# Kernel tuning notes

Hardware: AMD Instinct MI355X
Metric: run time of the kernel (lower is better)

The kernel has to match this reference:

```python
import jax, jax.numpy as jnp
import numpy as np

# structural constants (from dg config / init_kwargs)
B = 8192      # batch (L=1)
N = 64        # number of columns
C = 16        # one-hot width per column
D = N * C     # 1024
NUM = 32      # first NUM columns are numeric (use info['range'])
NCAUSAL = 16  # causal_cols = range(16)
K = 8         # info['range'][i] is [C, K]
HS = 1024
HP = 1024
TAU = 0.7
SMOOTH = 0.1  # kwargs['smoothing']


def setup_inputs() -> dict:
    key = jax.random.key(0)
    ks = jax.random.split(key, 20)
    s = 0.02
    inp = {
        'x': jax.random.uniform(ks[0], (B, D), dtype=jnp.float32),
        'truth_x': jax.random.normal(ks[1], (B, N), dtype=jnp.float32),
        # selector: Linear(D,HS) -> ReLU -> Linear(HS,N) -> Sigmoid
        'sel_w1': jax.random.normal(ks[2], (D, HS)) * s,
        'sel_b1': jnp.zeros((HS,), jnp.float32),
        'sel_w2': jax.random.normal(ks[3], (HS, N)) * s,
        'sel_b2': jnp.zeros((N,), jnp.float32),
        # perturber: D->HP->HP->HP->D with ReLU between
        'pw1': jax.random.normal(ks[4], (D, HP)) * s,
        'pb1': jnp.zeros((HP,), jnp.float32),
        'pw2': jax.random.normal(ks[5], (HP, HP)) * s,
        'pb2': jnp.zeros((HP,), jnp.float32),
        'pw3': jax.random.normal(ks[6], (HP, HP)) * s,
        'pb3': jnp.zeros((HP,), jnp.float32),
        'pw4': jax.random.normal(ks[7], (HP, D)) * s,
        'pb4': jnp.zeros((D,), jnp.float32),
        # dg.info['range'][i] for numeric columns: [NUM, C, K]
        'ranges': jax.random.normal(ks[8], (NUM, C, K), dtype=jnp.float32),
        # pre-drawn noise (training branch)
        'unif_a': jax.random.uniform(ks[9], (B, N), minval=1e-6, maxval=1.0 - 1e-6),
        'unif_b': jax.random.uniform(ks[10], (B, N), minval=1e-6, maxval=1.0 - 1e-6),
        'gumbel': jax.random.gumbel(ks[11], (B, N, C), dtype=jnp.float32),
    }
    return inp


def reference(x, truth_x, sel_w1, sel_b1, sel_w2, sel_b2,
              pw1, pb1, pw2, pb2, pw3, pb3, pw4, pb4,
              ranges, unif_a, unif_b, gumbel):
    # selector -> P in (0,1), shape [B, N]
    P = jax.nn.sigmoid(jax.nn.relu(x @ sel_w1 + sel_b1) @ sel_w2 + sel_b2)
    # relaxed Bernoulli (Sample_Bernoulli, training branch)
    ga = -jnp.log(-jnp.log(unif_a))
    gb = -jnp.log(-jnp.log(unif_b))
    no_logits = P * jnp.exp(ga) / TAU
    de_logits = no_logits + (1.0 - P) * jnp.exp(gb) / TAU
    probs = no_logits / de_logits                       # [B, N]
    # perturber MLP -> W, shape [B, D]
    h = jax.nn.relu(x @ pw1 + pb1)
    h = jax.nn.relu(h @ pw2 + pb2)
    h = jax.nn.relu(h @ pw3 + pb3)
    W = h @ pw4 + pb4
    # per-column blocks
    xr = x.reshape(B, N, C)
    logits = W.reshape(B, N, C)
    # data-dependent causal masking for causal columns
    curr = jnp.argmax(xr, axis=-1)                      # [B, N]
    causal = (jnp.arange(N) < NCAUSAL)[None, :, None]   # [1, N, 1]
    below = jnp.arange(C)[None, None, :] < curr[:, :, None]
    mask = jnp.where(causal & below, -100.0, jnp.where(causal, 1.0, 0.0))
    logits = logits + mask
    # label smoothing then Gumbel-softmax (soft), per Sample_Categorical
    pr = jax.nn.softmax(logits, axis=-1)
    pr = (1.0 - SMOOTH) * pr + SMOOTH / C
    logits = jnp.log(pr)
    y = jax.nn.softmax((logits + gumbel) / TAU, axis=-1)  # [B, N, C]
    # numeric columns: map categorical sample through range table, mix with truth
    xt_num = jnp.einsum('bnc,nck->bnk', y[:, :NUM], ranges).mean(axis=-1)  # [B, NUM]
    p_num = probs[:, :NUM]
    out_num = p_num * xt_num + (1.0 - p_num) * truth_x[:, :NUM]           # [B, NUM]
    # categorical columns: mix relaxed sample with original one-hot block
    p_cat = probs[:, NUM:, None]
    out_cat = p_cat * y[:, NUM:] + (1.0 - p_cat) * xr[:, NUM:]            # [B, N-NUM, C]
    xcf = jnp.concatenate([out_num, out_cat.reshape(B, (N - NUM) * C)], axis=1)
    return truth_x, xcf, P, W
```

## Files before the change

kernel.cpp:

```cpp
#include <hip/hip_runtime.h>
#include <hip/hip_bf16.h>
#include <cstdint>

#define B_DIM 8192
#define N_DIM 64
#define C_DIM 16
#define D_DIM 1024
#define NUM 32
#define NCAUSAL 16
#define K_RANGES 8
#define HS 1024
#define HP 1024
#define TAU 0.7f
#define SMOOTH 0.1f

typedef __bf16 bf16x8 __attribute__((ext_vector_type(8)));
typedef float f32x16 __attribute__((ext_vector_type(16)));

typedef const __attribute__((address_space(1))) uint32_t* gas_ptr;
typedef __attribute__((address_space(3))) uint32_t* las_ptr;

__device__ __forceinline__ void gld_lds16(const void* g, void* l) {
    __builtin_amdgcn_global_load_lds((gas_ptr)(uintptr_t)g,
                                     (las_ptr)(uint32_t)(uintptr_t)l,
                                     16, 0, 0);
}

__device__ __forceinline__ int swz(int r) { return (r & 3) ^ ((r >> 2) & 3); }

template <int ACT>
__device__ __forceinline__ void gemm_body2(
    const ushort* __restrict__ Ag, const ushort* __restrict__ Bg,
    const float* __restrict__ bias,
    float* __restrict__ Cf, __hip_bfloat16* __restrict__ Cb,
    int lda, int Nout, int ldC, int K, long m0, long n0,
    uint4 (*As)[512], uint4 (*Bs)[512])
{
    const int tid  = threadIdx.x;
    const int wave = tid >> 6;
    const int lane = tid & 63;
    const int wr = wave >> 1, wc = wave & 1;
    const int ln31 = lane & 31, blk = lane >> 5;

    f32x16 acc[2][2];
#pragma unroll
    for (int i = 0; i < 2; ++i)
#pragma unroll
        for (int j = 0; j < 2; ++j) acc[i][j] = (f32x16)(0.0f);

    const int c0 = wave * 128 + lane;
    const int c1 = wave * 128 + 64 + lane;

#define ISSUE_STAGE(buf, kt)                                                   \
    {                                                                          \
        int r0 = c0 >> 2, kc0 = (c0 & 3) ^ swz(r0);                            \
        int r1 = c1 >> 2, kc1 = (c1 & 3) ^ swz(r1);                            \
        gld_lds16(Ag + (m0 + r0) * (long)lda + (kt) + kc0 * 8,                 \
                  &As[buf][wave * 128]);                                       \
        gld_lds16(Bg + (n0 + r0) * (long)K + (kt) + kc0 * 8,                   \
                  &Bs[buf][wave * 128]);                                       \
        gld_lds16(Ag + (m0 + r1) * (long)lda + (kt) + kc1 * 8,                 \
                  &As[buf][wave * 128 + 64]);                                  \
        gld_lds16(Bg + (n0 + r1) * (long)K + (kt) + kc1 * 8,                   \
                  &Bs[buf][wave * 128 + 64]);                                  \
    }

    ISSUE_STAGE(0, 0);
    int cur = 0;
    for (int kt = 0; kt < K; kt += 32) {
        __syncthreads();
        if (kt + 32 < K) ISSUE_STAGE(cur ^ 1, kt + 32);

        bf16x8 af[2][2], bfr[2][2];
#pragma unroll
        for (int ks = 0; ks < 2; ++ks) {
            int ch = ks * 2 + blk;
#pragma unroll
            for (int mi = 0; mi < 2; ++mi) {
                int r = wr * 64 + mi * 32 + ln31;
                af[ks][mi] = __builtin_bit_cast(bf16x8, As[cur][r * 4 + (ch ^ swz(r))]);
            }
#pragma unroll
            for (int ni = 0; ni < 2; ++ni) {
                int n = wc * 64 + ni * 32 + ln31;
                bfr[ks][ni] = __builtin_bit_cast(bf16x8, Bs[cur][n * 4 + (ch ^ swz(n))]);
            }
        }
#pragma unroll
        for (int ks = 0; ks < 2; ++ks)
#pragma unroll
            for (int mi = 0; mi < 2; ++mi)
#pragma unroll
                for (int ni = 0; ni < 2; ++ni)
                    acc[mi][ni] = __builtin_amdgcn_mfma_f32_32x32x16_bf16(
                        af[ks][mi], bfr[ks][ni], acc[mi][ni], 0, 0, 0);
        cur ^= 1;
    }
#undef ISSUE_STAGE

    float bs2[2];
#pragma unroll
    for (int ni = 0; ni < 2; ++ni) {
        long col = n0 + wc * 64 + ni * 32 + ln31;
        bs2[ni] = (col < Nout && bias) ? bias[col] : 0.0f;
    }

#pragma unroll
    for (int mi = 0; mi < 2; ++mi) {
#pragma unroll
        for (int ni = 0; ni < 2; ++ni) {
            long col = n0 + wc * 64 + ni * 32 + ln31;
            if (col >= Nout) continue;
#pragma unroll
            for (int reg = 0; reg < 16; ++reg) {
                long row = m0 + wr * 64 + mi * 32 + (reg & 3) + 8 * (reg >> 2) + 4 * blk;
                float v = acc[mi][ni][reg] + bs2[ni];
                if (ACT == 1) {
                    v = fmaxf(v, 0.0f);
                    Cb[row * (long)ldC + col] = __float2bfloat16(v);
                } else if (ACT == 2) {
                    v = 1.0f / (1.0f + __expf(-v));
                    Cf[row * (long)ldC + col] = v;
                } else {
                    Cf[row * (long)ldC + col] = v;
                }
            }
        }
    }
}

template <int ACT>
__global__ __launch_bounds__(256, 2) void gemm_bt4(
    const __hip_bfloat16* __restrict__ A, const __hip_bfloat16* __restrict__ Bt,
    const float* __restrict__ bias,
    float* __restrict__ Cf, __hip_bfloat16* __restrict__ Cb,
    int lda, int Nout, int ldC, int K)
{
    __shared__ uint4 As[1024];
    __shared__ uint4 Bs[512];

    const ushort* Ag = (const ushort*)A;
    const ushort* Bg = (const ushort*)Bt;
    const long m0 = (long)blockIdx.y * 256;
    const long n0 = (long)blockIdx.x * 128;

    const int tid  = threadIdx.x;
    const int wave = tid >> 6;
    const int lane = tid & 63;
    const int wr = wave >> 1, wc = wave & 1;
    const int ln31 = lane & 31, blk = lane >> 5;

    f32x16 acc[4][2];
#pragma unroll
    for (int i = 0; i < 4; ++i)
#pragma unroll
        for (int j = 0; j < 2; ++j) acc[i][j] = (f32x16)(0.0f);

    for (int kt = 0; kt < K; kt += 32) {
#pragma unroll
        for (int r = 0; r < 4; ++r) {
            int s = r * 256 + tid;
            int row = s >> 2, ch = (s & 3) ^ swz(row);
            gld_lds16(Ag + (m0 + row) * (long)lda + kt + ch * 8,
                      &As[r * 256 + (wave << 6)]);
        }
#pragma unroll
        for (int r = 0; r < 2; ++r) {
            int s = r * 256 + tid;
            int row = s >> 2, ch = (s & 3) ^ swz(row);
            gld_lds16(Bg + (n0 + row) * (long)K + kt + ch * 8,
                      &Bs[r * 256 + (wave << 6)]);
        }
        __syncthreads();

        bf16x8 af[2][4], bfr[2][2];
#pragma unroll
        for (int ks = 0; ks < 2; ++ks) {
            int ch = ks * 2 + blk;
#pragma unroll
            for (int mi = 0; mi < 4; ++mi) {
                int r_ = wr * 128 + mi * 32 + ln31;
                af[ks][mi] = __builtin_bit_cast(bf16x8, As[r_ * 4 + (ch ^ swz(r_))]);
            }
#pragma unroll
            for (int ni = 0; ni < 2; ++ni) {
                int n_ = wc * 64 + ni * 32 + ln31;
                bfr[ks][ni] = __builtin_bit_cast(bf16x8, Bs[n_ * 4 + (ch ^ swz(n_))]);
            }
        }
#pragma unroll
        for (int ks = 0; ks < 2; ++ks)
#pragma unroll
            for (int mi = 0; mi < 4; ++mi)
#pragma unroll
                for (int ni = 0; ni < 2; ++ni)
                    acc[mi][ni] = __builtin_amdgcn_mfma_f32_32x32x16_bf16(
                        af[ks][mi], bfr[ks][ni], acc[mi][ni], 0, 0, 0);

        __syncthreads();
    }

    float bs2[2];
#pragma unroll
    for (int ni = 0; ni < 2; ++ni) {
        long col = n0 + wc * 64 + ni * 32 + ln31;
        bs2[ni] = (col < Nout && bias) ? bias[col] : 0.0f;
    }

#pragma unroll
    for (int mi = 0; mi < 4; ++mi) {
#pragma unroll
        for (int ni = 0; ni < 2; ++ni) {
            long col = n0 + wc * 64 + ni * 32 + ln31;
            if (col >= Nout) continue;
#pragma unroll
            for (int reg = 0; reg < 16; ++reg) {
                long row = m0 + wr * 128 + mi * 32 + (reg & 3) + 8 * (reg >> 2) + 4 * blk;
                float v = acc[mi][ni][reg] + bs2[ni];
                if (ACT == 1) {
                    v = fmaxf(v, 0.0f);
                    Cb[row * (long)ldC + col] = __float2bfloat16(v);
                } else if (ACT == 2) {
                    v = 1.0f / (1.0f + __expf(-v));
                    Cf[row * (long)ldC + col] = v;
                } else {
                    Cf[row * (long)ldC + col] = v;
                }
            }
        }
    }
}

template <int ACT>
__global__ __launch_bounds__(256, 2) void gemm_bt2(
    const __hip_bfloat16* __restrict__ A, const __hip_bfloat16* __restrict__ Bt,
    const float* __restrict__ bias,
    float* __restrict__ Cf, __hip_bfloat16* __restrict__ Cb,
    int lda, int Nout, int ldC, int K)
{
    __shared__ uint4 As[2][512];
    __shared__ uint4 Bs[2][512];
    gemm_body2<ACT>((const ushort*)A, (const ushort*)Bt, bias, Cf, Cb,
                    lda, Nout, ldC, K,
                    (long)blockIdx.y * 128, (long)blockIdx.x * 128, As, Bs);
}

__global__ __launch_bounds__(256, 2) void gemm_fused23(
    const __hip_bfloat16* __restrict__ act1,
    const __hip_bfloat16* __restrict__ p2t, const float* __restrict__ pb2,
    __hip_bfloat16* __restrict__ actB,
    const __hip_bfloat16* __restrict__ w2t, const float* __restrict__ sel_b2,
    float* __restrict__ outP)
{
    __shared__ uint4 As[2][512];
    __shared__ uint4 Bs[2][512];
    long m0 = (long)blockIdx.y * 128;
    if (blockIdx.x < 8) {
        gemm_body2<1>((const ushort*)(act1 + 1024), (const ushort*)p2t, pb2,
                      nullptr, actB, 2048, 1024, 1024, 1024,
                      m0, (long)blockIdx.x * 128, As, Bs);
    } else {
        gemm_body2<2>((const ushort*)act1, (const ushort*)w2t, sel_b2,
                      outP, nullptr, 2048, 64, 64, 1024,
                      m0, 0, As, Bs);
    }
}

struct PrepArgs {
    const float* src[6];
    __hip_bfloat16* dst[6];
    int Nsrc[6];
    int Npad[6];
    const float* ranges; float* rmean;
    const float* b1; const float* b2; float* bcat;
    const float* x; __hip_bfloat16* xbf;
};

__global__ void prep_kernel(PrepArgs a)
{
    int z = blockIdx.z;
    int tx = threadIdx.x, ty = threadIdx.y;
    int t = ty * 32 + tx;
    if (z == 7) {
        int bid = blockIdx.y * 32 + blockIdx.x;
        const float4* s4 = (const float4*)a.x;
        for (int i = bid * 256 + t; i < B_DIM * D_DIM / 4; i += 1024 * 256) {
            float4 v = s4[i];
            __hip_bfloat16* d = a.xbf + (size_t)i * 4;
            d[0] = __float2bfloat16(v.x);
            d[1] = __float2bfloat16(v.y);
            d[2] = __float2bfloat16(v.z);
            d[3] = __float2bfloat16(v.w);
        }
        return;
    }
    if (z == 6) {
        if (blockIdx.x || blockIdx.y) return;
        for (int j = t; j < NUM * C_DIM; j += 256) {
            float s = 0.0f;
#pragma unroll
            for (int k = 0; k < K_RANGES; ++k) s += a.ranges[j * K_RANGES + k];
            a.rmean[j] = s * (1.0f / K_RANGES);
        }
        for (int j = t; j < 1024; j += 256) {
            a.bcat[j]        = a.b1[j];
            a.bcat[1024 + j] = a.b2[j];
        }
        return;
    }
    const int Nsrc = a.Nsrc[z], Npad = a.Npad[z];
    int n0 = blockIdx.x * 32, k0 = blockIdx.y * 32;
    if (n0 >= Npad) return;
    const float* src = a.src[z];
    __hip_bfloat16* dst = a.dst[z];
    __shared__ float tile[32][33];
#pragma unroll
    for (int i = 0; i < 32; i += 8) {
        int k = k0 + ty + i, n = n0 + tx;
        tile[ty + i][tx] = (n < Nsrc) ? src[(size_t)k * Nsrc + n] : 0.0f;
    }
    __syncthreads();
#pragma unroll
    for (int i = 0; i < 32; i += 8) {
        int n = n0 + ty + i, k = k0 + tx;
        dst[(size_t)n * D_DIM + k] = __float2bfloat16(tile[tx][ty + i]);
    }
}

__global__ void finalize_kernel(
    const float* __restrict__ x, const float* __restrict__ truth,
    const float* __restrict__ ua, const float* __restrict__ ub,
    const float* __restrict__ gum, const float* __restrict__ rmean,
    const float* __restrict__ P, const float* __restrict__ W,
    float* __restrict__ out_truth, float* __restrict__ out_xcf)
{
    int idx = blockIdx.x * 256 + threadIdx.x;
    if (idx >= B_DIM * N_DIM) return;
    int b = idx >> 6, n = idx & 63;

    float tx = truth[idx];
    out_truth[idx] = tx;

    float p  = P[idx];
    float ea = -1.0f / logf(ua[idx]);
    float eb = -1.0f / logf(ub[idx]);
    float no = p * ea;
    float probs = no / (no + (1.0f - p) * eb);

    const float* Wrow = W + (size_t)idx * 16;
    const float* grow = gum + (size_t)idx * 16;
    float lo[16], g[16], xv[16];
#pragma unroll
    for (int c = 0; c < 16; c += 4) {
        float4 v = *(const float4*)(Wrow + c);
        lo[c] = v.x; lo[c + 1] = v.y; lo[c + 2] = v.z; lo[c + 3] = v.w;
        float4 gv = *(const float4*)(grow + c);
        g[c] = gv.x; g[c + 1] = gv.y; g[c + 2] = gv.z; g[c + 3] = gv.w;
    }

    bool needx = (n < NCAUSAL) || (n >= NUM);
    if (needx) {
        const float* xrow = x + (size_t)idx * 16;
#pragma unroll
        for (int c = 0; c < 16; c += 4) {
            float4 v = *(const float4*)(xrow + c);
            xv[c] = v.x; xv[c + 1] = v.y; xv[c + 2] = v.z; xv[c + 3] = v.w;
        }
    }

    if (n < NCAUSAL) {
        int curr = 0; float best = xv[0];
#pragma unroll
        for (int c = 1; c < 16; ++c)
            if (xv[c] > best) { best = xv[c]; curr = c; }
#pragma unroll
        for (int c = 0; c < 16; ++c) lo[c] += (c < curr) ? -100.0f : 1.0f;
    }

    float mx = lo[0];
#pragma unroll
    for (int c = 1; c < 16; ++c) mx = fmaxf(mx, lo[c]);
    float s = 0.0f, pr[16];
#pragma unroll
    for (int c = 0; c < 16; ++c) { pr[c] = __expf(lo[c] - mx); s += pr[c]; }
    float inv = 1.0f / s;
#pragma unroll
    for (int c = 0; c < 16; ++c)
        pr[c] = (1.0f - SMOOTH) * pr[c] * inv + (SMOOTH / C_DIM);

    float t[16];
    float mx2 = -1e30f;
#pragma unroll
    for (int c = 0; c < 16; ++c) {
        t[c] = (__logf(pr[c]) + g[c]) * (1.0f / TAU);
        mx2 = fmaxf(mx2, t[c]);
    }
    float s2 = 0.0f;
#pragma unroll
    for (int c = 0; c < 16; ++c) { t[c] = __expf(t[c] - mx2); s2 += t[c]; }
    float inv2 = 1.0f / s2;

    if (n < NUM) {
        float xt = 0.0f;
#pragma unroll
        for (int c = 0; c < 16; ++c) xt += t[c] * inv2 * rmean[n * 16 + c];
        out_xcf[(size_t)b * 544 + n] = probs * xt + (1.0f - probs) * tx;
    } else {
        float* o = out_xcf + (size_t)b * 544 + 32 + (size_t)(n - NUM) * 16;
#pragma unroll
        for (int c = 0; c < 16; ++c)
            o[c] = probs * t[c] * inv2 + (1.0f - probs) * xv[c];
    }
}

extern "C" void kernel_launch(void* const* d_in, const int* in_sizes, int n_in,
                              void* d_out, int out_size, void* d_ws, size_t ws_size,
                              hipStream_t stream)
{
    const float* x      = (const float*)d_in[0];
    const float* truth  = (const float*)d_in[1];
    const float* sel_w1 = (const float*)d_in[2];
    const float* sel_b1 = (const float*)d_in[3];
    const float* sel_w2 = (const float*)d_in[4];
    const float* sel_b2 = (const float*)d_in[5];
    const float* pw1    = (const float*)d_in[6];
    const float* pb1    = (const float*)d_in[7];
    const float* pw2    = (const float*)d_in[8];
    const float* pb2    = (const float*)d_in[9];
    const float* pw3    = (const float*)d_in[10];
    const float* pb3    = (const float*)d_in[11];
    const float* pw4    = (const float*)d_in[12];
    const float* pb4    = (const float*)d_in[13];
    const float* ranges = (const float*)d_in[14];
    const float* ua     = (const float*)d_in[15];
    const float* ub     = (const float*)d_in[16];
    const float* gum    = (const float*)d_in[17];

    float* out       = (float*)d_out;
    float* out_truth = out;
    float* out_xcf   = out + 524288;
    float* out_P     = out + 4980736;
    float* out_W     = out + 5505024;

    char* w = (char*)d_ws;
    size_t off = 0;
    __hip_bfloat16* A0   = (__hip_bfloat16*)(w + off); off += (size_t)B_DIM * D_DIM * 2;
    __hip_bfloat16* act1 = (__hip_bfloat16*)(w + off); off += (size_t)B_DIM * 2048 * 2;
    __hip_bfloat16* actB = (__hip_bfloat16*)(w + off); off += (size_t)B_DIM * HP * 2;
    __hip_bfloat16* actC = (__hip_bfloat16*)(w + off); off += (size_t)B_DIM * HP * 2;
    __hip_bfloat16* Wcat = (__hip_bfloat16*)(w + off); off += (size_t)2048 * D_DIM * 2;
    __hip_bfloat16* w2t  = (__hip_bfloat16*)(w + off); off += (size_t)128 * HS * 2;
    __hip_bfloat16* p2t  = (__hip_bfloat16*)(w + off); off += (size_t)HP * HP * 2;
    __hip_bfloat16* p3t  = (__hip_bfloat16*)(w + off); off += (size_t)HP * HP * 2;
    __hip_bfloat16* p4t  = (__hip_bfloat16*)(w + off); off += (size_t)D_DIM * HP * 2;
    float* rmean         = (float*)(w + off);          off += 512 * 4;
    float* bcat          = (float*)(w + off);          off += 2048 * 4;
    if (ws_size < off) return;

    PrepArgs pa;
    pa.src[0] = sel_w1; pa.dst[0] = Wcat;               pa.Nsrc[0] = HS;    pa.Npad[0] = 1024;
    pa.src[1] = pw1;    pa.dst[1] = Wcat + 1024 * 1024; pa.Nsrc[1] = HP;    pa.Npad[1] = 1024;
    pa.src[2] = sel_w2; pa.dst[2] = w2t;                pa.Nsrc[2] = N_DIM; pa.Npad[2] = 128;
    pa.src[3] = pw2;    pa.dst[3] = p2t;                pa.Nsrc[3] = HP;    pa.Npad[3] = 1024;
    pa.src[4] = pw3;    pa.dst[4] = p3t;                pa.Nsrc[4] = HP;    pa.Npad[4] = 1024;
    pa.src[5] = pw4;    pa.dst[5] = p4t;                pa.Nsrc[5] = D_DIM; pa.Npad[5] = 1024;
    pa.ranges = ranges; pa.rmean = rmean;
    pa.b1 = sel_b1; pa.b2 = pb1; pa.bcat = bcat;
    pa.x = x; pa.xbf = A0;

    prep_kernel<<<dim3(32, 32, 8), dim3(32, 8), 0, stream>>>(pa);

    gemm_bt4<1><<<dim3(16, 32), 256, 0, stream>>>(A0, Wcat, bcat, nullptr, act1,
                                                  D_DIM, 2048, 2048, D_DIM);
    gemm_fused23<<<dim3(9, 64), 256, 0, stream>>>(act1, p2t, pb2, actB, w2t, sel_b2, out_P);
    gemm_bt2<1><<<dim3(8, 64), 256, 0, stream>>>(actB, p3t, pb3, nullptr, actC,
                                                 HP, HP, HP, HP);
    gemm_bt2<0><<<dim3(8, 64), 256, 0, stream>>>(actC, p4t, pb4, out_W, nullptr,
                                                 HP, D_DIM, D_DIM, HP);

    finalize_kernel<<<(B_DIM * N_DIM + 255) / 256, 256, 0, stream>>>(
        x, truth, ua, ub, gum, rmean, out_P, out_W, out_truth, out_xcf);
}
```

Baseline: 303.5 us.

## Replace GEMM kernels with 256x256 8-wave pipelined GEMM and regroup selector layer

Replaces the separate 128/256-row GEMM kernels with a single 512-thread kernel that computes 256x256 tiles with K-step 64, an 8-chunk XOR swizzle, staged prefetch interleaved across four MFMA phases with explicit vmcnt waits, barriers and s_setprio, plus an XCD-aware block index swizzle. The selector second layer is moved from the layer-2 launch into the layer-3 launch as a second part, with its weight padding raised to 256 rows. The aim is higher data reuse per tile and better overlap of global-to-LDS loads with MFMA work. In exchange, grids shrink to 128-256 workgroups (wave quantization on many CUs), the tiles need more registers, and the padded selector part does wasted work.

```diff
diff --git a/kernel.cpp b/kernel.cpp
--- a/kernel.cpp
+++ b/kernel.cpp
@@ -26,244 +26,188 @@
                                      16, 0, 0);
 }
 
-__device__ __forceinline__ int swz(int r) { return (r & 3) ^ ((r >> 2) & 3); }
-
-template <int ACT>
-__device__ __forceinline__ void gemm_body2(
-    const ushort* __restrict__ Ag, const ushort* __restrict__ Bg,
-    const float* __restrict__ bias,
-    float* __restrict__ Cf, __hip_bfloat16* __restrict__ Cb,
-    int lda, int Nout, int ldC, int K, long m0, long n0,
-    uint4 (*As)[512], uint4 (*Bs)[512])
+struct G8Part {
+    const ushort* A; const ushort* B; const float* bias;
+    float* Cf; __hip_bfloat16* Cb;
+    int act, lda, Nout, ldC;
+};
+struct G8Args { G8Part p[2]; int K, split; };
+
+__device__ __forceinline__ void gemm8_body(
+    const G8Part& P, int K, long m0, long n0, uint4* lds)
 {
+    const ushort* __restrict__ Ag = P.A;
+    const ushort* __restrict__ Bg = P.B;
+    const int lda = P.lda;
+
     const int tid  = threadIdx.x;
     const int wave = tid >> 6;
     const int lane = tid & 63;
-    const int wr = wave >> 1, wc = wave & 1;
+    const int wr = wave >> 2, wcn = wave & 3;
     const int ln31 = lane & 31, blk = lane >> 5;
-
-    f32x16 acc[2][2];
-#pragma unroll
-    for (int i = 0; i < 2; ++i)
+    const int sl = (wave << 6) + lane;
+    const int nt = K >> 6;
+
+    uint4* Alds = lds;
+    uint4* Blds = lds + 4096;
+
+#define STAGE_A(buf, qoff, kt)                                                 \
+    {                                                                          \
+        _Pragma("unroll")                                                      \
+        for (int i_ = 0; i_ < 2; ++i_) {                                       \
+            int r_  = (i_ << 7) + (qoff) + (sl >> 3);                          \
+            int c_  = sl & 7;                                                  \
+            int gk_ = (kt) + ((c_ ^ (r_ & 7)) << 3);                           \
+            gld_lds16(Ag + (m0 + r_) * (long)lda + gk_,                        \
+                      Alds + (buf) * 2048 + (((i_ << 7) + (qoff)) << 3) +      \
+                          (wave << 6));                                        \
+        }                                                                      \
+    }
+#define STAGE_B(buf, h, kt)                                                    \
+    {                                                                          \
+        _Pragma("unroll")                                                      \
+        for (int i_ = 0; i_ < 2; ++i_) {                                       \
+            int r_  = ((h) << 7) + (i_ << 6) + (sl >> 3);                      \
+            int c_  = sl & 7;                                                  \
+            int gk_ = (kt) + ((c_ ^ (r_ & 7)) << 3);                           \
+            gld_lds16(Bg + (n0 + r_) * (long)K + gk_,                          \
+                      Blds + (buf) * 2048 + ((((h) << 7) + (i_ << 6)) << 3) +  \
+                          (wave << 6));                                        \
+        }                                                                      \
+    }
+#define LDA_F(buf, mi)                                                         \
+    _Pragma("unroll")                                                          \
+    for (int ks_ = 0; ks_ < 4; ++ks_) {                                        \
+        int r_ = wr * 128 + (mi) * 32 + ln31;                                  \
+        int c_ = (ks_ * 2 + blk) ^ (r_ & 7);                                   \
+        aF[ks_] = __builtin_bit_cast(bf16x8, Alds[(buf) * 2048 + r_ * 8 + c_]);\
+    }
+#define LDB_F(buf)                                                             \
+    _Pragma("unroll")                                                          \
+    for (int ni_ = 0; ni_ < 2; ++ni_) {                                        \
+        _Pragma("unroll")                                                      \
+        for (int ks_ = 0; ks_ < 4; ++ks_) {                                    \
+            int r_ = wcn * 64 + ni_ * 32 + ln31;                               \
+            int c_ = (ks_ * 2 + blk) ^ (r_ & 7);                               \
+            bF[ni_][ks_] =                                                     \
+                __builtin_bit_cast(bf16x8, Blds[(buf) * 2048 + r_ * 8 + c_]);  \
+        }                                                                      \
+    }
+#define PHASE_MFMA(mi)                                                         \
+    __builtin_amdgcn_s_barrier();                                              \
+    asm volatile("s_waitcnt lgkmcnt(0)");                                      \
+    __builtin_amdgcn_s_setprio(1);                                             \
+    _Pragma("unroll")                                                          \
+    for (int ks_ = 0; ks_ < 4; ++ks_) {                                        \
+        _Pragma("unroll")                                                      \
+        for (int ni_ = 0; ni_ < 2; ++ni_)                                      \
+            acc[mi][ni_] = __builtin_amdgcn_mfma_f32_32x32x16_bf16(            \
+                aF[ks_], bF[ni_][ks_], acc[mi][ni_], 0, 0, 0);                 \
+    }                                                                          \
+    __builtin_amdgcn_s_setprio(0);                                             \
+    __builtin_amdgcn_s_barrier();
+
+    STAGE_A(0, 0, 0);
+    STAGE_A(0, 64, 0);
+    STAGE_B(0, 0, 0);
+    STAGE_B(0, 1, 0);
+    STAGE_B(1, 0, 64);
+    STAGE_B(1, 1, 64);
+    STAGE_A(1, 0, 64);
+    asm volatile("s_waitcnt vmcnt(6)");
+    __builtin_amdgcn_s_barrier();
+
+    f32x16 acc[4][2];
+#pragma unroll
+    for (int i = 0; i < 4; ++i)
 #pragma unroll
         for (int j = 0; j < 2; ++j) acc[i][j] = (f32x16)(0.0f);
 
-    const int c0 = wave * 128 + lane;
-    const int c1 = wave * 128 + 64 + lane;
-
-#define ISSUE_STAGE(buf, kt)                                                   \
-    {                                                                          \
-        int r0 = c0 >> 2, kc0 = (c0 & 3) ^ swz(r0);                            \
-        int r1 = c1 >> 2, kc1 = (c1 & 3) ^ swz(r1);                            \
-        gld_lds16(Ag + (m0 + r0) * (long)lda + (kt) + kc0 * 8,                 \
-                  &As[buf][wave * 128]);                                       \
-        gld_lds16(Bg + (n0 + r0) * (long)K + (kt) + kc0 * 8,                   \
-                  &Bs[buf][wave * 128]);                                       \
-        gld_lds16(Ag + (m0 + r1) * (long)lda + (kt) + kc1 * 8,                 \
-                  &As[buf][wave * 128 + 64]);                                  \
-        gld_lds16(Bg + (n0 + r1) * (long)K + (kt) + kc1 * 8,                   \
-                  &Bs[buf][wave * 128 + 64]);                                  \
-    }
-
-    ISSUE_STAGE(0, 0);
-    int cur = 0;
-    for (int kt = 0; kt < K; kt += 32) {
-        __syncthreads();
-        if (kt + 32 < K) ISSUE_STAGE(cur ^ 1, kt + 32);
-
-        bf16x8 af[2][2], bfr[2][2];
-#pragma unroll
-        for (int ks = 0; ks < 2; ++ks) {
-            int ch = ks * 2 + blk;
-#pragma unroll
-            for (int mi = 0; mi < 2; ++mi) {
-                int r = wr * 64 + mi * 32 + ln31;
-                af[ks][mi] = __builtin_bit_cast(bf16x8, As[cur][r * 4 + (ch ^ swz(r))]);
-            }
-#pragma unroll
-            for (int ni = 0; ni < 2; ++ni) {
-                int n = wc * 64 + ni * 32 + ln31;
-                bfr[ks][ni] = __builtin_bit_cast(bf16x8, Bs[cur][n * 4 + (ch ^ swz(n))]);
-            }
-        }
-#pragma unroll
-        for (int ks = 0; ks < 2; ++ks)
-#pragma unroll
-            for (int mi = 0; mi < 2; ++mi)
-#pragma unroll
-                for (int ni = 0; ni < 2; ++ni)
-                    acc[mi][ni] = __builtin_amdgcn_mfma_f32_32x32x16_bf16(
-                        af[ks][mi], bfr[ks][ni], acc[mi][ni], 0, 0, 0);
-        cur ^= 1;
-    }
-#undef ISSUE_STAGE
-
+    for (int t = 0; t < nt; ++t) {
+        const int buf = t & 1;
+        bf16x8 aF[4], bF[2][4];
+
+        LDB_F(buf);
+        LDA_F(buf, 0);
+        if (t + 1 < nt) STAGE_A(buf ^ 1, 64, (t + 1) << 6);
+        PHASE_MFMA(0);
+
+        LDA_F(buf, 1);
+        if (t + 2 < nt) STAGE_B(buf, 0, (t + 2) << 6);
+        PHASE_MFMA(1);
+
+        LDA_F(buf, 2);
+        if (t + 2 < nt) STAGE_B(buf, 1, (t + 2) << 6);
+        PHASE_MFMA(2);
+
+        LDA_F(buf, 3);
+        if (t + 2 < nt) STAGE_A(buf, 0, (t + 2) << 6);
+        if (t < nt - 2) {
+            asm volatile("s_waitcnt vmcnt(6)");
+        } else if (t == nt - 2) {
+            asm volatile("s_waitcnt vmcnt(0)");
+        }
+        PHASE_MFMA(3);
+    }
+#undef STAGE_A
+#undef STAGE_B
+#undef LDA_F
+#undef LDB_F
+#undef PHASE_MFMA
+
+    const int act = P.act, Nout = P.Nout, ldC = P.ldC;
     float bs2[2];
 #pragma unroll
     for (int ni = 0; ni < 2; ++ni) {
-        long col = n0 + wc * 64 + ni * 32 + ln31;
-        bs2[ni] = (col < Nout && bias) ? bias[col] : 0.0f;
-    }
-
-#pragma unroll
-    for (int mi = 0; mi < 2; ++mi) {
+        long col = n0 + wcn * 64 + ni * 32 + ln31;
+        bs2[ni] = (col < Nout && P.bias) ? P.bias[col] : 0.0f;
+    }
+#pragma unroll
+    for (int mi = 0; mi < 4; ++mi) {
 #pragma unroll
         for (int ni = 0; ni < 2; ++ni) {
-            long col = n0 + wc * 64 + ni * 32 + ln31;
-            if (col >= Nout) continue;
-#pragma unroll
-            for (int reg = 0; reg < 16; ++reg) {
-                long row = m0 + wr * 64 + mi * 32 + (reg & 3) + 8 * (reg >> 2) + 4 * blk;
-                float v = acc[mi][ni][reg] + bs2[ni];
-                if (ACT == 1) {
-                    v = fmaxf(v, 0.0f);
-                    Cb[row * (long)ldC + col] = __float2bfloat16(v);
-                } else if (ACT == 2) {
-                    v = 1.0f / (1.0f + __expf(-v));
-                    Cf[row * (long)ldC + col] = v;
-                } else {
-                    Cf[row * (long)ldC + col] = v;
-                }
-            }
-        }
-    }
-}
-
-template <int ACT>
-__global__ __launch_bounds__(256, 2) void gemm_bt4(
-    const __hip_bfloat16* __restrict__ A, const __hip_bfloat16* __restrict__ Bt,
-    const float* __restrict__ bias,
-    float* __restrict__ Cf, __hip_bfloat16* __restrict__ Cb,
-    int lda, int Nout, int ldC, int K)
-{
-    __shared__ uint4 As[1024];
-    __shared__ uint4 Bs[512];
-
-    const ushort* Ag = (const ushort*)A;
-    const ushort* Bg = (const ushort*)Bt;
-    const long m0 = (long)blockIdx.y * 256;
-    const long n0 = (long)blockIdx.x * 128;
-
-    const int tid  = threadIdx.x;
-    const int wave = tid >> 6;
-    const int lane = tid & 63;
-    const int wr = wave >> 1, wc = wave & 1;
-    const int ln31 = lane & 31, blk = lane >> 5;
-
-    f32x16 acc[4][2];
-#pragma unroll
-    for (int i = 0; i < 4; ++i)
-#pragma unroll
-        for (int j = 0; j < 2; ++j) acc[i][j] = (f32x16)(0.0f);
-
-    for (int kt = 0; kt < K; kt += 32) {
-#pragma unroll
-        for (int r = 0; r < 4; ++r) {
-            int s = r * 256 + tid;
-            int row = s >> 2, ch = (s & 3) ^ swz(row);
-            gld_lds16(Ag + (m0 + row) * (long)lda + kt + ch * 8,
-                      &As[r * 256 + (wave << 6)]);
-        }
-#pragma unroll
-        for (int r = 0; r < 2; ++r) {
-            int s = r * 256 + tid;
-            int row = s >> 2, ch = (s & 3) ^ swz(row);
-            gld_lds16(Bg + (n0 + row) * (long)K + kt + ch * 8,
-                      &Bs[r * 256 + (wave << 6)]);
-        }
-        __syncthreads();
-
-        bf16x8 af[2][4], bfr[2][2];
-#pragma unroll
-        for (int ks = 0; ks < 2; ++ks) {
-            int ch = ks * 2 + blk;
-#pragma unroll
-            for (int mi = 0; mi < 4; ++mi) {
-                int r_ = wr * 128 + mi * 32 + ln31;
-                af[ks][mi] = __builtin_bit_cast(bf16x8, As[r_ * 4 + (ch ^ swz(r_))]);
-            }
-#pragma unroll
-            for (int ni = 0; ni < 2; ++ni) {
-                int n_ = wc * 64 + ni * 32 + ln31;
-                bfr[ks][ni] = __builtin_bit_cast(bf16x8, Bs[n_ * 4 + (ch ^ swz(n_))]);
-            }
-        }
-#pragma unroll
-        for (int ks = 0; ks < 2; ++ks)
-#pragma unroll
-            for (int mi = 0; mi < 4; ++mi)
-#pragma unroll
-                for (int ni = 0; ni < 2; ++ni)
-                    acc[mi][ni] = __builtin_amdgcn_mfma_f32_32x32x16_bf16(
-                        af[ks][mi], bfr[ks][ni], acc[mi][ni], 0, 0, 0);
-
-        __syncthreads();
-    }
-
-    float bs2[2];
-#pragma unroll
-    for (int ni = 0; ni < 2; ++ni) {
-        long col = n0 + wc * 64 + ni * 32 + ln31;
-        bs2[ni] = (col < Nout && bias) ? bias[col] : 0.0f;
-    }
-
-#pragma unroll
-    for (int mi = 0; mi < 4; ++mi) {
-#pragma unroll
-        for (int ni = 0; ni < 2; ++ni) {
-            long col = n0 + wc * 64 + ni * 32 + ln31;
+            long col = n0 + wcn * 64 + ni * 32 + ln31;
             if (col >= Nout) continue;
 #pragma unroll
             for (int reg = 0; reg < 16; ++reg) {
                 long row = m0 + wr * 128 + mi * 32 + (reg & 3) + 8 * (reg >> 2) + 4 * blk;
                 float v = acc[mi][ni][reg] + bs2[ni];
-                if (ACT == 1) {
+                if (act == 1) {
                     v = fmaxf(v, 0.0f);
-                    Cb[row * (long)ldC + col] = __float2bfloat16(v);
-                } else if (ACT == 2) {
+                    P.Cb[row * (long)ldC + col] = __float2bfloat16(v);
+                } else if (act == 2) {
                     v = 1.0f / (1.0f + __expf(-v));
-                    Cf[row * (long)ldC + col] = v;
+                    P.Cf[row * (long)ldC + col] = v;
                 } else {
-                    Cf[row * (long)ldC + col] = v;
+                    P.Cf[row * (long)ldC + col] = v;
                 }
             }
         }
     }
 }
 
-template <int ACT>
-__global__ __launch_bounds__(256, 2) void gemm_bt2(
-    const __hip_bfloat16* __restrict__ A, const __hip_bfloat16* __restrict__ Bt,
-    const float* __restrict__ bias,
-    float* __restrict__ Cf, __hip_bfloat16* __restrict__ Cb,
-    int lda, int Nout, int ldC, int K)
+__global__ __launch_bounds__(512, 2) void gemm8_k(G8Args g)
 {
-    __shared__ uint4 As[2][512];
-    __shared__ uint4 Bs[2][512];
-    gemm_body2<ACT>((const ushort*)A, (const ushort*)Bt, bias, Cf, Cb,
-                    lda, Nout, ldC, K,
-                    (long)blockIdx.y * 128, (long)blockIdx.x * 128, As, Bs);
-}
-
-__global__ __launch_bounds__(256, 2) void gemm_fused23(
-    const __hip_bfloat16* __restrict__ act1,
-    const __hip_bfloat16* __restrict__ p2t, const float* __restrict__ pb2,
-    __hip_bfloat16* __restrict__ actB,
-    const __hip_bfloat16* __restrict__ w2t, const float* __restrict__ sel_b2,
-    float* __restrict__ outP)
-{
-    __shared__ uint4 As[2][512];
-    __shared__ uint4 Bs[2][512];
-    long m0 = (long)blockIdx.y * 128;
-    if (blockIdx.x < 8) {
-        gemm_body2<1>((const ushort*)(act1 + 1024), (const ushort*)p2t, pb2,
-                      nullptr, actB, 2048, 1024, 1024, 1024,
-                      m0, (long)blockIdx.x * 128, As, Bs);
+    __shared__ uint4 lds[8192];
+    const int nwg = gridDim.x;
+    const int cpx = nwg >> 3;
+    const int bid = blockIdx.x;
+    const int swz = (bid & 7) * cpx + (bid >> 3);
+
+    long m0, n0;
+    int part;
+    if (swz < g.split) {
+        part = 0;
+        int ty = swz & 31;
+        int tx = swz >> 5;
+        m0 = (long)ty * 256;
+        n0 = (long)tx * 256;
     } else {
-        gemm_body2<2>((const ushort*)act1, (const ushort*)w2t, sel_b2,
-                      outP, nullptr, 2048, 64, 64, 1024,
-                      m0, 0, As, Bs);
-    }
+        part = 1;
+        m0 = (long)(swz - g.split) * 256;
+        n0 = 0;
+    }
+    gemm8_body(g.p[part], g.K, m0, n0, lds);
 }
 
 struct PrepArgs {
@@ -449,7 +393,7 @@
     __hip_bfloat16* actB = (__hip_bfloat16*)(w + off); off += (size_t)B_DIM * HP * 2;
     __hip_bfloat16* actC = (__hip_bfloat16*)(w + off); off += (size_t)B_DIM * HP * 2;
     __hip_bfloat16* Wcat = (__hip_bfloat16*)(w + off); off += (size_t)2048 * D_DIM * 2;
-    __hip_bfloat16* w2t  = (__hip_bfloat16*)(w + off); off += (size_t)128 * HS * 2;
+    __hip_bfloat16* w2t  = (__hip_bfloat16*)(w + off); off += (size_t)256 * HS * 2;
     __hip_bfloat16* p2t  = (__hip_bfloat16*)(w + off); off += (size_t)HP * HP * 2;
     __hip_bfloat16* p3t  = (__hip_bfloat16*)(w + off); off += (size_t)HP * HP * 2;
     __hip_bfloat16* p4t  = (__hip_bfloat16*)(w + off); off += (size_t)D_DIM * HP * 2;
@@ -460,7 +404,7 @@
     PrepArgs pa;
     pa.src[0] = sel_w1; pa.dst[0] = Wcat;               pa.Nsrc[0] = HS;    pa.Npad[0] = 1024;
     pa.src[1] = pw1;    pa.dst[1] = Wcat + 1024 * 1024; pa.Nsrc[1] = HP;    pa.Npad[1] = 1024;
-    pa.src[2] = sel_w2; pa.dst[2] = w2t;                pa.Nsrc[2] = N_DIM; pa.Npad[2] = 128;
+    pa.src[2] = sel_w2; pa.dst[2] = w2t;                pa.Nsrc[2] = N_DIM; pa.Npad[2] = 256;
     pa.src[3] = pw2;    pa.dst[3] = p2t;                pa.Nsrc[3] = HP;    pa.Npad[3] = 1024;
     pa.src[4] = pw3;    pa.dst[4] = p3t;                pa.Nsrc[4] = HP;    pa.Npad[4] = 1024;
     pa.src[5] = pw4;    pa.dst[5] = p4t;                pa.Nsrc[5] = D_DIM; pa.Npad[5] = 1024;
@@ -470,13 +414,36 @@
 
     prep_kernel<<<dim3(32, 32, 8), dim3(32, 8), 0, stream>>>(pa);
 
-    gemm_bt4<1><<<dim3(16, 32), 256, 0, stream>>>(A0, Wcat, bcat, nullptr, act1,
-                                                  D_DIM, 2048, 2048, D_DIM);
-    gemm_fused23<<<dim3(9, 64), 256, 0, stream>>>(act1, p2t, pb2, actB, w2t, sel_b2, out_P);
-    gemm_bt2<1><<<dim3(8, 64), 256, 0, stream>>>(actB, p3t, pb3, nullptr, actC,
-                                                 HP, HP, HP, HP);
-    gemm_bt2<0><<<dim3(8, 64), 256, 0, stream>>>(actC, p4t, pb4, out_W, nullptr,
-                                                 HP, D_DIM, D_DIM, HP);
+    {
+        G8Args g{};
+        g.p[0] = { (const ushort*)A0, (const ushort*)Wcat, bcat,
+                   nullptr, act1, 1, 1024, 2048, 2048 };
+        g.K = 1024; g.split = 256;
+        gemm8_k<<<256, 512, 0, stream>>>(g);
+    }
+    {
+        G8Args g{};
+        g.p[0] = { (const ushort*)(act1 + 1024), (const ushort*)p2t, pb2,
+                   nullptr, actB, 1, 2048, 1024, 1024 };
+        g.K = 1024; g.split = 128;
+        gemm8_k<<<128, 512, 0, stream>>>(g);
+    }
+    {
+        G8Args g{};
+        g.p[0] = { (const ushort*)actB, (const ushort*)p3t, pb3,
+                   nullptr, actC, 1, 1024, 1024, 1024 };
+        g.p[1] = { (const ushort*)act1, (const ushort*)w2t, sel_b2,
+                   out_P, nullptr, 2, 2048, 64, 64 };
+        g.K = 1024; g.split = 128;
+        gemm8_k<<<160, 512, 0, stream>>>(g);
+    }
+    {
+        G8Args g{};
+        g.p[0] = { (const ushort*)actC, (const ushort*)p4t, pb4,
+                   out_W, nullptr, 0, 1024, 1024, 1024 };
+        g.K = 1024; g.split = 128;
+        gemm8_k<<<128, 512, 0, stream>>>(g);
+    }
 
     finalize_kernel<<<(B_DIM * N_DIM + 255) / 256, 256, 0, stream>>>(
         x, truth, ua, ub, gum, rmean, out_P, out_W, out_truth, out_xcf);
```

Measured after the change: 360.1 us. +18.7%, slower.

## Use 8-wave 128x128 GEMM blocks with one load per thread per stage

Applied to the files above, without the earlier changes.

Rewrites the GEMM body so each 128x128 tile is computed by 8 waves, where each wave owns a 64x32 sub-tile, instead of 4 waves each owning 64x64. Each thread now issues a single A and B async load per stage, and the load addresses are precomputed once. The first GEMM switches from the 256x128 single-buffered kernel to this double-buffered 128x128 kernel. The aim is more resident waves per CU to hide latency, fewer accumulator registers, and cheaper address math. In exchange, each wave reuses its fragments less, so the LDS read traffic per MFMA goes up.

```diff
diff --git a/kernel.cpp b/kernel.cpp
--- a/kernel.cpp
+++ b/kernel.cpp
@@ -29,7 +29,7 @@
 __device__ __forceinline__ int swz(int r) { return (r & 3) ^ ((r >> 2) & 3); }
 
 template <int ACT>
-__device__ __forceinline__ void gemm_body2(
+__device__ __forceinline__ void gemm_body8(
     const ushort* __restrict__ Ag, const ushort* __restrict__ Bg,
     const float* __restrict__ bias,
     float* __restrict__ Cf, __hip_bfloat16* __restrict__ Cb,
@@ -38,91 +38,70 @@
 {
     const int tid  = threadIdx.x;
     const int wave = tid >> 6;
-    const int lane = tid & 63;
-    const int wr = wave >> 1, wc = wave & 1;
-    const int ln31 = lane & 31, blk = lane >> 5;
-
-    f32x16 acc[2][2];
-#pragma unroll
-    for (int i = 0; i < 2; ++i)
-#pragma unroll
-        for (int j = 0; j < 2; ++j) acc[i][j] = (f32x16)(0.0f);
-
-    const int c0 = wave * 128 + lane;
-    const int c1 = wave * 128 + 64 + lane;
-
-#define ISSUE_STAGE(buf, kt)                                                   \
+    const int ln31 = tid & 31, blk = (tid >> 5) & 1;
+    const int wr = wave >> 2, wc = wave & 3;
+
+    const int row = tid >> 2;
+    const int ch  = (tid & 3) ^ swz(row);
+    const ushort* aSrc = Ag + (m0 + row) * (long)lda + ch * 8;
+    const ushort* bSrc = Bg + (n0 + row) * (long)K   + ch * 8;
+    const int ldsOff = wave << 6;
+
+    f32x16 acc[2];
+    acc[0] = (f32x16)(0.0f);
+    acc[1] = (f32x16)(0.0f);
+
+#define ISSUE_STAGE8(buf, kt)                                                  \
     {                                                                          \
-        int r0 = c0 >> 2, kc0 = (c0 & 3) ^ swz(r0);                            \
-        int r1 = c1 >> 2, kc1 = (c1 & 3) ^ swz(r1);                            \
-        gld_lds16(Ag + (m0 + r0) * (long)lda + (kt) + kc0 * 8,                 \
-                  &As[buf][wave * 128]);                                       \
-        gld_lds16(Bg + (n0 + r0) * (long)K + (kt) + kc0 * 8,                   \
-                  &Bs[buf][wave * 128]);                                       \
-        gld_lds16(Ag + (m0 + r1) * (long)lda + (kt) + kc1 * 8,                 \
-                  &As[buf][wave * 128 + 64]);                                  \
-        gld_lds16(Bg + (n0 + r1) * (long)K + (kt) + kc1 * 8,                   \
-                  &Bs[buf][wave * 128 + 64]);                                  \
-    }
-
-    ISSUE_STAGE(0, 0);
+        gld_lds16(aSrc + (kt), &As[buf][ldsOff]);                              \
+        gld_lds16(bSrc + (kt), &Bs[buf][ldsOff]);                              \
+    }
+
+    ISSUE_STAGE8(0, 0);
     int cur = 0;
     for (int kt = 0; kt < K; kt += 32) {
         __syncthreads();
-        if (kt + 32 < K) ISSUE_STAGE(cur ^ 1, kt + 32);
-
-        bf16x8 af[2][2], bfr[2][2];
+        if (kt + 32 < K) ISSUE_STAGE8(cur ^ 1, kt + 32);
+
+        bf16x8 af[2][2], bfr[2];
 #pragma unroll
         for (int ks = 0; ks < 2; ++ks) {
-            int ch = ks * 2 + blk;
+            int c = ks * 2 + blk;
 #pragma unroll
             for (int mi = 0; mi < 2; ++mi) {
                 int r = wr * 64 + mi * 32 + ln31;
-                af[ks][mi] = __builtin_bit_cast(bf16x8, As[cur][r * 4 + (ch ^ swz(r))]);
+                af[ks][mi] = __builtin_bit_cast(bf16x8, As[cur][r * 4 + (c ^ swz(r))]);
             }
-#pragma unroll
-            for (int ni = 0; ni < 2; ++ni) {
-                int n = wc * 64 + ni * 32 + ln31;
-                bfr[ks][ni] = __builtin_bit_cast(bf16x8, Bs[cur][n * 4 + (ch ^ swz(n))]);
-            }
+            int n = wc * 32 + ln31;
+            bfr[ks] = __builtin_bit_cast(bf16x8, Bs[cur][n * 4 + (c ^ swz(n))]);
         }
 #pragma unroll
         for (int ks = 0; ks < 2; ++ks)
 #pragma unroll
             for (int mi = 0; mi < 2; ++mi)
-#pragma unroll
-                for (int ni = 0; ni < 2; ++ni)
-                    acc[mi][ni] = __builtin_amdgcn_mfma_f32_32x32x16_bf16(
-                        af[ks][mi], bfr[ks][ni], acc[mi][ni], 0, 0, 0);
+                acc[mi] = __builtin_amdgcn_mfma_f32_32x32x16_bf16(
+                    af[ks][mi], bfr[ks], acc[mi], 0, 0, 0);
         cur ^= 1;
     }
-#undef ISSUE_STAGE
-
-    float bs2[2];
-#pragma unroll
-    for (int ni = 0; ni < 2; ++ni) {
-        long col = n0 + wc * 64 + ni * 32 + ln31;
-        bs2[ni] = (col < Nout && bias) ? bias[col] : 0.0f;
-    }
-
-#pragma unroll
-    for (int mi = 0; mi < 2; ++mi) {
-#pragma unroll
-        for (int ni = 0; ni < 2; ++ni) {
-            long col = n0 + wc * 64 + ni * 32 + ln31;
-            if (col >= Nout) continue;
+#undef ISSUE_STAGE8
+
+    long col = n0 + wc * 32 + ln31;
+    if (col < Nout) {
+        float bs = bias ? bias[col] : 0.0f;
+#pragma unroll
+        for (int mi = 0; mi < 2; ++mi) {
 #pragma unroll
             for (int reg = 0; reg < 16; ++reg) {
-                long row = m0 + wr * 64 + mi * 32 + (reg & 3) + 8 * (reg >> 2) + 4 * blk;
-                float v = acc[mi][ni][reg] + bs2[ni];
+                long r2 = m0 + wr * 64 + mi * 32 + (reg & 3) + 8 * (reg >> 2) + 4 * blk;
+                float v = acc[mi][reg] + bs;
                 if (ACT == 1) {
                     v = fmaxf(v, 0.0f);
-                    Cb[row * (long)ldC + col] = __float2bfloat16(v);
+                    Cb[r2 * (long)ldC + col] = __float2bfloat16(v);
                 } else if (ACT == 2) {
                     v = 1.0f / (1.0f + __expf(-v));
-                    Cf[row * (long)ldC + col] = v;
+                    Cf[r2 * (long)ldC + col] = v;
                 } else {
-                    Cf[row * (long)ldC + col] = v;
+                    Cf[r2 * (long)ldC + col] = v;
                 }
             }
         }
@@ -130,122 +109,20 @@
 }
 
 template <int ACT>
-__global__ __launch_bounds__(256, 2) void gemm_bt4(
+__global__ __launch_bounds__(512, 4) void gemm8(
     const __hip_bfloat16* __restrict__ A, const __hip_bfloat16* __restrict__ Bt,
     const float* __restrict__ bias,
     float* __restrict__ Cf, __hip_bfloat16* __restrict__ Cb,
     int lda, int Nout, int ldC, int K)
 {
-    __shared__ uint4 As[1024];
-    __shared__ uint4 Bs[512];
-
-    const ushort* Ag = (const ushort*)A;
-    const ushort* Bg = (const ushort*)Bt;
-    const long m0 = (long)blockIdx.y * 256;
-    const long n0 = (long)blockIdx.x * 128;
-
-    const int tid  = threadIdx.x;
-    const int wave = tid >> 6;
-    const int lane = tid & 63;
-    const int wr = wave >> 1, wc = wave & 1;
-    const int ln31 = lane & 31, blk = lane >> 5;
-
-    f32x16 acc[4][2];
-#pragma unroll
-    for (int i = 0; i < 4; ++i)
-#pragma unroll
-        for (int j = 0; j < 2; ++j) acc[i][j] = (f32x16)(0.0f);
-
-    for (int kt = 0; kt < K; kt += 32) {
-#pragma unroll
-        for (int r = 0; r < 4; ++r) {
-            int s = r * 256 + tid;
-            int row = s >> 2, ch = (s & 3) ^ swz(row);
-            gld_lds16(Ag + (m0 + row) * (long)lda + kt + ch * 8,
-                      &As[r * 256 + (wave << 6)]);
-        }
-#pragma unroll
-        for (int r = 0; r < 2; ++r) {
-            int s = r * 256 + tid;
-            int row = s >> 2, ch = (s & 3) ^ swz(row);
-            gld_lds16(Bg + (n0 + row) * (long)K + kt + ch * 8,
-                      &Bs[r * 256 + (wave << 6)]);
-        }
-        __syncthreads();
-
-        bf16x8 af[2][4], bfr[2][2];
-#pragma unroll
-        for (int ks = 0; ks < 2; ++ks) {
-            int ch = ks * 2 + blk;
-#pragma unroll
-            for (int mi = 0; mi < 4; ++mi) {
-                int r_ = wr * 128 + mi * 32 + ln31;
-                af[ks][mi] = __builtin_bit_cast(bf16x8, As[r_ * 4 + (ch ^ swz(r_))]);
-            }
-#pragma unroll
-            for (int ni = 0; ni < 2; ++ni) {
-                int n_ = wc * 64 + ni * 32 + ln31;
-                bfr[ks][ni] = __builtin_bit_cast(bf16x8, Bs[n_ * 4 + (ch ^ swz(n_))]);
-            }
-        }
-#pragma unroll
-        for (int ks = 0; ks < 2; ++ks)
-#pragma unroll
-            for (int mi = 0; mi < 4; ++mi)
-#pragma unroll
-                for (int ni = 0; ni < 2; ++ni)
-                    acc[mi][ni] = __builtin_amdgcn_mfma_f32_32x32x16_bf16(
-                        af[ks][mi], bfr[ks][ni], acc[mi][ni], 0, 0, 0);
-
-        __syncthreads();
-    }
-
-    float bs2[2];
-#pragma unroll
-    for (int ni = 0; ni < 2; ++ni) {
-        long col = n0 + wc * 64 + ni * 32 + ln31;
-        bs2[ni] = (col < Nout && bias) ? bias[col] : 0.0f;
-    }
-
-#pragma unroll
-    for (int mi = 0; mi < 4; ++mi) {
-#pragma unroll
-        for (int ni = 0; ni < 2; ++ni) {
-            long col = n0 + wc * 64 + ni * 32 + ln31;
-            if (col >= Nout) continue;
-#pragma unroll
-            for (int reg = 0; reg < 16; ++reg) {
-                long row = m0 + wr * 128 + mi * 32 + (reg & 3) + 8 * (reg >> 2) + 4 * blk;
-                float v = acc[mi][ni][reg] + bs2[ni];
-                if (ACT == 1) {
-                    v = fmaxf(v, 0.0f);
-                    Cb[row * (long)ldC + col] = __float2bfloat16(v);
-                } else if (ACT == 2) {
-                    v = 1.0f / (1.0f + __expf(-v));
-                    Cf[row * (long)ldC + col] = v;
-                } else {
-                    Cf[row * (long)ldC + col] = v;
-                }
-            }
-        }
-    }
-}
-
-template <int ACT>
-__global__ __launch_bounds__(256, 2) void gemm_bt2(
-    const __hip_bfloat16* __restrict__ A, const __hip_bfloat16* __restrict__ Bt,
-    const float* __restrict__ bias,
-    float* __restrict__ Cf, __hip_bfloat16* __restrict__ Cb,
-    int lda, int Nout, int ldC, int K)
-{
     __shared__ uint4 As[2][512];
     __shared__ uint4 Bs[2][512];
-    gemm_body2<ACT>((const ushort*)A, (const ushort*)Bt, bias, Cf, Cb,
+    gemm_body8<ACT>((const ushort*)A, (const ushort*)Bt, bias, Cf, Cb,
                     lda, Nout, ldC, K,
                     (long)blockIdx.y * 128, (long)blockIdx.x * 128, As, Bs);
 }
 
-__global__ __launch_bounds__(256, 2) void gemm_fused23(
+__global__ __launch_bounds__(512, 4) void gemm8_fused23(
     const __hip_bfloat16* __restrict__ act1,
     const __hip_bfloat16* __restrict__ p2t, const float* __restrict__ pb2,
     __hip_bfloat16* __restrict__ actB,
@@ -256,11 +133,11 @@
     __shared__ uint4 Bs[2][512];
     long m0 = (long)blockIdx.y * 128;
     if (blockIdx.x < 8) {
-        gemm_body2<1>((const ushort*)(act1 + 1024), (const ushort*)p2t, pb2,
+        gemm_body8<1>((const ushort*)(act1 + 1024), (const ushort*)p2t, pb2,
                       nullptr, actB, 2048, 1024, 1024, 1024,
                       m0, (long)blockIdx.x * 128, As, Bs);
     } else {
-        gemm_body2<2>((const ushort*)act1, (const ushort*)w2t, sel_b2,
+        gemm_body8<2>((const ushort*)act1, (const ushort*)w2t, sel_b2,
                       outP, nullptr, 2048, 64, 64, 1024,
                       m0, 0, As, Bs);
     }
@@ -470,13 +347,14 @@
 
     prep_kernel<<<dim3(32, 32, 8), dim3(32, 8), 0, stream>>>(pa);
 
-    gemm_bt4<1><<<dim3(16, 32), 256, 0, stream>>>(A0, Wcat, bcat, nullptr, act1,
-                                                  D_DIM, 2048, 2048, D_DIM);
-    gemm_fused23<<<dim3(9, 64), 256, 0, stream>>>(act1, p2t, pb2, actB, w2t, sel_b2, out_P);
-    gemm_bt2<1><<<dim3(8, 64), 256, 0, stream>>>(actB, p3t, pb3, nullptr, actC,
-                                                 HP, HP, HP, HP);
-    gemm_bt2<0><<<dim3(8, 64), 256, 0, stream>>>(actC, p4t, pb4, out_W, nullptr,
-                                                 HP, D_DIM, D_DIM, HP);
+    gemm8<1><<<dim3(16, 64), 512, 0, stream>>>(A0, Wcat, bcat, nullptr, act1,
+                                               D_DIM, 2048, 2048, D_DIM);
+    gemm8_fused23<<<dim3(9, 64), 512, 0, stream>>>(act1, p2t, pb2, actB, w2t,
+                                                   sel_b2, out_P);
+    gemm8<1><<<dim3(8, 64), 512, 0, stream>>>(actB, p3t, pb3, nullptr, actC,
+                                              HP, HP, HP, HP);
+    gemm8<0><<<dim3(8, 64), 512, 0, stream>>>(actC, p4t, pb4, out_W, nullptr,
+                                              HP, D_DIM, D_DIM, HP);
 
     finalize_kernel<<<(B_DIM * N_DIM + 255) / 256, 256, 0, stream>>>(
         x, truth, ua, ub, gum, rmean, out_P, out_W, out_truth, out_xcf);
```

New measurement: 306.3 us. About the same (+0.9%).
